# Optimization experiments

Measured on AMD Instinct MI355X. Metric: run time of the kernel, lower is better.

Reference implementation:

```python
import jax, jax.numpy as jnp
import numpy as np

N, IN_DIM, H1, H2, LIN, MAX_INDEX = 16384, 64, 256, 256, 64, 256


def _init_layer(key, out_dim, in_dim):
    # mimic kaiming_uniform(a=sqrt(5)) + uniform bias bound = 1/sqrt(fan_in)
    kW, kb = jax.random.split(key)
    bound_w = 1.0 / np.sqrt(in_dim)  # gain*sqrt(3/fan_in) with a=sqrt(5) -> 1/sqrt(fan_in)
    W = jax.random.uniform(kW, (MAX_INDEX, out_dim, in_dim), jnp.float32, -bound_w, bound_w)
    b = jax.random.uniform(kb, (MAX_INDEX, out_dim), jnp.float32, -bound_w, bound_w)
    return W, b


def setup_inputs() -> dict:
    key = jax.random.key(0)
    kx, ki, k1, k2, k3 = jax.random.split(key, 5)
    x = jax.random.normal(kx, (N, IN_DIM), jnp.float32)
    ind = jax.random.randint(ki, (N,), 0, MAX_INDEX, jnp.int64 if jax.config.jax_enable_x64 else jnp.int32)
    W1, b1 = _init_layer(k1, H1, IN_DIM)
    W2, b2 = _init_layer(k2, H2, H1)
    Wl, bl = _init_layer(k3, LIN, H2)
    return {"x": x, "ind": ind, "W1": W1, "b1": b1, "W2": W2, "b2": b2, "Wl": Wl, "bl": bl}


def _index_linear(x, ind, W, b):
    # per-row expert weight gather then row-wise matvec: out[n] = W[ind[n]] @ x[n] + b[ind[n]]
    return jnp.einsum('noi,ni->no', W[ind], x) + b[ind]


def reference(x, ind, W1, b1, W2, b2, Wl, bl):
    h = jnp.tanh(_index_linear(x, ind, W1, b1))
    h = jnp.tanh(_index_linear(h, ind, W2, b2))
    return _index_linear(h, ind, Wl, bl)
```

## Files before the change

kernel.cpp:

```cpp
#include <hip/hip_runtime.h>
#include <math.h>

#define NROWS   16384
#define IN_DIM  64
#define HID     256
#define OUT_DIM 64
#define NEXP    256
#define MT      112
#define NT      7
#define HP      264

typedef __attribute__((ext_vector_type(8))) short short8;
typedef __attribute__((ext_vector_type(4))) float f32x4;
typedef __attribute__((ext_vector_type(4))) unsigned uint4v;
typedef __attribute__((ext_vector_type(2))) unsigned uint2v;

#define LBAR() do { \
    asm volatile("s_waitcnt lgkmcnt(0)" ::: "memory"); \
    __builtin_amdgcn_s_barrier(); } while (0)


__global__ __launch_bounds__(256) void hist_k(const int* __restrict__ ind,
                                              int* __restrict__ hist) {
  int n = blockIdx.x * 256 + threadIdx.x;
  atomicAdd(&hist[ind[n]], 1);
}

__global__ __launch_bounds__(256) void scan_k(const int* __restrict__ hist,
                                              int* __restrict__ offsets,
                                              int* __restrict__ cur) {
  __shared__ int s[NEXP];
  int t = threadIdx.x;
  int h = hist[t];
  s[t] = h;
  __syncthreads();
  for (int d = 1; d < NEXP; d <<= 1) {
    int v = (t >= d) ? s[t - d] : 0;
    __syncthreads();
    s[t] += v;
    __syncthreads();
  }
  int exc = s[t] - h;
  offsets[t] = exc;
  cur[t] = exc;
  if (t == NEXP - 1) offsets[NEXP] = s[t];
}

__global__ __launch_bounds__(256) void scatter_k(const int* __restrict__ ind,
                                                 int* __restrict__ cur,
                                                 int* __restrict__ rows) {
  int n = blockIdx.x * 256 + threadIdx.x;
  int p = atomicAdd(&cur[ind[n]], 1);
  rows[p] = n;
}


__device__ __forceinline__ unsigned bf16_rn(float f) {
  unsigned u = __builtin_bit_cast(unsigned, f);
  unsigned r = 0x7fffu + ((u >> 16) & 1u);
  return (u + r) >> 16;
}

__device__ __forceinline__ unsigned pk2(float a, float b) {
  return bf16_rn(a) | (bf16_rn(b) << 16);
}

__device__ __forceinline__ short8 cvt8(f32x4 w0, f32x4 w1) {
  uint4v u;
  u.x = pk2(w0.x, w0.y);
  u.y = pk2(w0.z, w0.w);
  u.z = pk2(w1.x, w1.y);
  u.w = pk2(w1.z, w1.w);
  return __builtin_bit_cast(short8, u);
}

__device__ __forceinline__ float fast_tanh(float v) {
  float e = __expf(2.f * v);
  return 1.f - 2.f * __builtin_amdgcn_rcpf(e + 1.f);
}


__device__ __forceinline__ void preload2(const float* bp0, const float* bp1,
                                         f32x4 (&p)[2][2]) {
  p[0][0] = *(const f32x4*)(bp0);
  p[0][1] = *(const f32x4*)(bp0 + 4);
  p[1][0] = *(const f32x4*)(bp1);
  p[1][1] = *(const f32x4*)(bp1 + 4);
}

__device__ __forceinline__ void layer1_direct(const float* bp0, const float* bp1,
                                              f32x4 (&pre)[2][2],
                                              const unsigned short* Hin,
                                              int l15, int q, f32x4 (&acc)[2][NT]) {
  f32x4 wp[2][2][2];
  wp[0][0][0] = pre[0][0]; wp[0][0][1] = pre[0][1];
  wp[0][1][0] = pre[1][0]; wp[0][1][1] = pre[1][1];
#pragma unroll
  for (int ks = 0; ks < 2; ks++) {
    const int cu = ks & 1;
    if (ks + 1 < 2) {
      wp[cu ^ 1][0][0] = *(const f32x4*)(bp0 + (ks + 1) * 32);
      wp[cu ^ 1][0][1] = *(const f32x4*)(bp0 + (ks + 1) * 32 + 4);
      wp[cu ^ 1][1][0] = *(const f32x4*)(bp1 + (ks + 1) * 32);
      wp[cu ^ 1][1][1] = *(const f32x4*)(bp1 + (ks + 1) * 32 + 4);
    }
    short8 a0 = cvt8(wp[cu][0][0], wp[cu][0][1]);
    short8 a1 = cvt8(wp[cu][1][0], wp[cu][1][1]);
#pragma unroll
    for (int nt = 0; nt < NT; nt++) {
      short8 b = *(const short8*)&Hin[(nt * 16 + l15) * HP + ks * 32 + q * 8];
      acc[0][nt] = __builtin_amdgcn_mfma_f32_16x16x32_bf16(a0, b, acc[0][nt], 0, 0, 0);
      acc[1][nt] = __builtin_amdgcn_mfma_f32_16x16x32_bf16(a1, b, acc[1][nt], 0, 0, 0);
    }
  }
}

__device__ __forceinline__ void layer2_direct(const float* bp0, const float* bp1,
                                              f32x4 (&pre)[2][2][2],
                                              const unsigned short* Hin,
                                              int l15, int q, f32x4 (&acc)[2][NT]) {
  f32x4 wp[3][2][2];
  wp[0][0][0] = pre[0][0][0]; wp[0][0][1] = pre[0][0][1];
  wp[0][1][0] = pre[0][1][0]; wp[0][1][1] = pre[0][1][1];
  wp[1][0][0] = pre[1][0][0]; wp[1][0][1] = pre[1][0][1];
  wp[1][1][0] = pre[1][1][0]; wp[1][1][1] = pre[1][1][1];
#pragma unroll
  for (int ks = 0; ks < 8; ks++) {
    const int cu = ks % 3;
    const int ld = (ks + 2) % 3;
    if (ks + 2 < 8) {
      wp[ld][0][0] = *(const f32x4*)(bp0 + (ks + 2) * 32);
      wp[ld][0][1] = *(const f32x4*)(bp0 + (ks + 2) * 32 + 4);
      wp[ld][1][0] = *(const f32x4*)(bp1 + (ks + 2) * 32);
      wp[ld][1][1] = *(const f32x4*)(bp1 + (ks + 2) * 32 + 4);
    }
    short8 a0 = cvt8(wp[cu][0][0], wp[cu][0][1]);
    short8 a1 = cvt8(wp[cu][1][0], wp[cu][1][1]);
#pragma unroll
    for (int nt = 0; nt < NT; nt++) {
      short8 b = *(const short8*)&Hin[(nt * 16 + l15) * HP + ks * 32 + q * 8];
      acc[0][nt] = __builtin_amdgcn_mfma_f32_16x16x32_bf16(a0, b, acc[0][nt], 0, 0, 0);
      acc[1][nt] = __builtin_amdgcn_mfma_f32_16x16x32_bf16(a1, b, acc[1][nt], 0, 0, 0);
    }
  }
}

__device__ __forceinline__ void layer3_direct(const float* bp, f32x4 (&pre)[2],
                                              const unsigned short* Hin,
                                              int w, int l15, int q,
                                              f32x4 (&accl)[4]) {
  f32x4 wp[2][2];
  wp[0][0] = pre[0]; wp[0][1] = pre[1];
#pragma unroll
  for (int kk = 0; kk < 8; kk++) {
    const int cu = kk & 1;
    if (kk + 1 < 8) {
      wp[cu ^ 1][0] = *(const f32x4*)(bp + (kk + 1) * 32);
      wp[cu ^ 1][1] = *(const f32x4*)(bp + (kk + 1) * 32 + 4);
    }
    short8 a = cvt8(wp[cu][0], wp[cu][1]);
#pragma unroll
    for (int i = 0; i < 4; i++) {
      int nt = (w >> 2) * 4 + i;
      if (nt < NT) {
        short8 b = *(const short8*)&Hin[(nt * 16 + l15) * HP + kk * 32 + q * 8];
        accl[i] = __builtin_amdgcn_mfma_f32_16x16x32_bf16(a, b, accl[i], 0, 0, 0);
      }
    }
  }
}

__device__ __forceinline__ void write_h8(f32x4 (&acc)[2][NT], unsigned short* Hd,
                                         int w, int l15, int q) {
#pragma unroll
  for (int mt = 0; mt < 2; mt++)
#pragma unroll
    for (int nt = 0; nt < NT; nt++) {
      uint2v v;
      v.x = pk2(fast_tanh(acc[mt][nt].x), fast_tanh(acc[mt][nt].y));
      v.y = pk2(fast_tanh(acc[mt][nt].z), fast_tanh(acc[mt][nt].w));
      *(uint2v*)&Hd[(nt * 16 + l15) * HP + w * 32 + mt * 16 + q * 4] = v;
    }
}


__global__ __launch_bounds__(512, 2) void mlp_k(
    const float* __restrict__ x,
    const float* __restrict__ W1, const float* __restrict__ b1,
    const float* __restrict__ W2, const float* __restrict__ b2,
    const float* __restrict__ Wl, const float* __restrict__ bl,
    const int* __restrict__ rows, const int* __restrict__ offsets,
    float* __restrict__ out) {
  __shared__ __align__(16) unsigned short H[MT * HP];

  const int t = threadIdx.x;
  const int w = t >> 6;
  const int l15 = t & 15;
  const int q = (t >> 4) & 3;
  const int e = blockIdx.x;
  const int beg = offsets[e];
  const int cnt = offsets[e + 1] - beg;

  const float* W1e = W1 + (size_t)e * HID * IN_DIM;
  const float* W2e = W2 + (size_t)e * HID * HID;
  const float* Wle = Wl + (size_t)e * OUT_DIM * HID;

  const float* bp1a = W1e + (size_t)(w * 32 + l15) * IN_DIM + q * 8;
  const float* bp1b = W1e + (size_t)(w * 32 + 16 + l15) * IN_DIM + q * 8;
  const float* bp2a = W2e + (size_t)(w * 32 + l15) * HID + q * 8;
  const float* bp2b = W2e + (size_t)(w * 32 + 16 + l15) * HID + q * 8;
  const float* bp3  = Wle + (size_t)((w & 3) * 16 + l15) * HID + q * 8;

  f32x4 b1v[2], b2v[2], blv;
#pragma unroll
  for (int mt = 0; mt < 2; mt++) {
    b1v[mt] = *(const f32x4*)(b1 + (size_t)e * HID + w * 32 + mt * 16 + q * 4);
    b2v[mt] = *(const f32x4*)(b2 + (size_t)e * HID + w * 32 + mt * 16 + q * 4);
  }
  blv = *(const f32x4*)(bl + (size_t)e * OUT_DIM + (w & 3) * 16 + q * 4);

  const int sr = t >> 2;
  const int sc = (t & 3) * 16;

  for (int mt0 = 0; mt0 < cnt; mt0 += MT) {
    f32x4 p1[2][2], p2[2][2][2], p3[2];
    preload2(bp1a, bp1b, p1);
    preload2(bp2a, bp2b, p2[0]);
    preload2(bp2a + 32, bp2b + 32, p2[1]);
    p3[0] = *(const f32x4*)(bp3);
    p3[1] = *(const f32x4*)(bp3 + 4);

    if (sr < MT) {
      int gm = mt0 + sr;
      bool val = gm < cnt;
      int r = val ? rows[beg + gm] : 0;
      const float* xr = x + (size_t)r * IN_DIM + sc;
      uint4v u0, u1;
      if (val) {
        f32x4 a0 = *(const f32x4*)(xr);
        f32x4 a1 = *(const f32x4*)(xr + 4);
        f32x4 a2 = *(const f32x4*)(xr + 8);
        f32x4 a3 = *(const f32x4*)(xr + 12);
        u0.x = pk2(a0.x, a0.y); u0.y = pk2(a0.z, a0.w);
        u0.z = pk2(a1.x, a1.y); u0.w = pk2(a1.z, a1.w);
        u1.x = pk2(a2.x, a2.y); u1.y = pk2(a2.z, a2.w);
        u1.z = pk2(a3.x, a3.y); u1.w = pk2(a3.z, a3.w);
      } else {
        u0 = (uint4v){0, 0, 0, 0};
        u1 = (uint4v){0, 0, 0, 0};
      }
      *(uint4v*)&H[sr * HP + sc] = u0;
      *(uint4v*)&H[sr * HP + sc + 8] = u1;
    }
    LBAR();

    f32x4 acc[2][NT];
#pragma unroll
    for (int mt = 0; mt < 2; mt++)
#pragma unroll
      for (int nt = 0; nt < NT; nt++) acc[mt][nt] = b1v[mt];
    layer1_direct(bp1a, bp1b, p1, H, l15, q, acc);
    LBAR();
    write_h8(acc, H, w, l15, q);
    LBAR();

#pragma unroll
    for (int mt = 0; mt < 2; mt++)
#pragma unroll
      for (int nt = 0; nt < NT; nt++) acc[mt][nt] = b2v[mt];
    layer2_direct(bp2a, bp2b, p2, H, l15, q, acc);
    LBAR();
    write_h8(acc, H, w, l15, q);
    LBAR();

    f32x4 accl[4];
#pragma unroll
    for (int i = 0; i < 4; i++) accl[i] = blv;
    layer3_direct(bp3, p3, H, w, l15, q, accl);

#pragma unroll
    for (int i = 0; i < 4; i++) {
      int nt = (w >> 2) * 4 + i;
      if (nt < NT) {
        int gm = mt0 + nt * 16 + l15;
        if (gm < cnt) {
          int r = rows[beg + gm];
          *(f32x4*)(out + (size_t)r * OUT_DIM + (w & 3) * 16 + q * 4) = accl[i];
        }
      }
    }
    LBAR();
  }
}


extern "C" void kernel_launch(void* const* d_in, const int* in_sizes, int n_in,
                              void* d_out, int out_size, void* d_ws, size_t ws_size,
                              hipStream_t stream) {
  const float* x   = (const float*)d_in[0];
  const int*   ind = (const int*)d_in[1];
  const float* W1  = (const float*)d_in[2];
  const float* b1  = (const float*)d_in[3];
  const float* W2  = (const float*)d_in[4];
  const float* b2  = (const float*)d_in[5];
  const float* Wl  = (const float*)d_in[6];
  const float* bl  = (const float*)d_in[7];
  float* out = (float*)d_out;

  int* offsets = (int*)d_ws;
  int* cur     = (int*)d_ws + 260;
  int* hist    = (int*)d_ws + 260;
  int* rows    = (int*)d_ws + 516;

  hipMemsetAsync(hist, 0, NEXP * sizeof(int), stream);
  hist_k<<<NROWS / 256, 256, 0, stream>>>(ind, hist);
  scan_k<<<1, 256, 0, stream>>>(hist, offsets, cur);
  scatter_k<<<NROWS / 256, 256, 0, stream>>>(ind, cur, rows);
  mlp_k<<<NEXP, 512, 0, stream>>>(x, W1, b1, W2, b2, Wl, bl, rows, offsets, out);
}
```

Baseline: 163.5 us.

## Use 16 waves per expert block, each owning 16 output rows

Doubles the block to 1024 threads (16 waves), so each wave computes a single 16-row slice of the hidden outputs instead of two 32-row tiles. The row tile grows from 112 to 128 so that the average of 64 rows per expert almost always fits in one tile. Weight register pressure per thread is halved and more waves hide global-load latency, but barrier costs grow with more waves. Each B fragment read from LDS is now reused by one MFMA instead of two, which doubles LDS read traffic per FLOP.

Result: slower. 169.1 us (+3.5%).

```diff
diff --git a/kernel.cpp b/kernel.cpp
--- a/kernel.cpp
+++ b/kernel.cpp
@@ -6,8 +6,8 @@
 #define HID     256
 #define OUT_DIM 64
 #define NEXP    256
-#define MT      112
-#define NT      7
+#define MT      128
+#define NT      8
 #define HP      264
 
 typedef __attribute__((ext_vector_type(8))) short short8;
@@ -80,77 +80,38 @@
 }
 
 
-__device__ __forceinline__ void preload2(const float* bp0, const float* bp1,
-                                         f32x4 (&p)[2][2]) {
-  p[0][0] = *(const f32x4*)(bp0);
-  p[0][1] = *(const f32x4*)(bp0 + 4);
-  p[1][0] = *(const f32x4*)(bp1);
-  p[1][1] = *(const f32x4*)(bp1 + 4);
-}
-
-__device__ __forceinline__ void layer1_direct(const float* bp0, const float* bp1,
-                                              f32x4 (&pre)[2][2],
-                                              const unsigned short* Hin,
-                                              int l15, int q, f32x4 (&acc)[2][NT]) {
-  f32x4 wp[2][2][2];
-  wp[0][0][0] = pre[0][0]; wp[0][0][1] = pre[0][1];
-  wp[0][1][0] = pre[1][0]; wp[0][1][1] = pre[1][1];
-#pragma unroll
-  for (int ks = 0; ks < 2; ks++) {
-    const int cu = ks & 1;
-    if (ks + 1 < 2) {
-      wp[cu ^ 1][0][0] = *(const f32x4*)(bp0 + (ks + 1) * 32);
-      wp[cu ^ 1][0][1] = *(const f32x4*)(bp0 + (ks + 1) * 32 + 4);
-      wp[cu ^ 1][1][0] = *(const f32x4*)(bp1 + (ks + 1) * 32);
-      wp[cu ^ 1][1][1] = *(const f32x4*)(bp1 + (ks + 1) * 32 + 4);
-    }
-    short8 a0 = cvt8(wp[cu][0][0], wp[cu][0][1]);
-    short8 a1 = cvt8(wp[cu][1][0], wp[cu][1][1]);
+template <int K>
+__device__ __forceinline__ void layerN(const float* bp, f32x4 (&pre)[2][2],
+                                       const unsigned short* Hin,
+                                       int l15, int q, f32x4 (&acc)[NT]) {
+  f32x4 wp[3][2];
+  wp[0][0] = pre[0][0]; wp[0][1] = pre[0][1];
+  wp[1][0] = pre[1][0]; wp[1][1] = pre[1][1];
+  constexpr int KS = K / 32;
+#pragma unroll
+  for (int ks = 0; ks < KS; ks++) {
+    const int cu = ks % 3;
+    const int ld = (ks + 2) % 3;
+    if (ks + 2 < KS) {
+      wp[ld][0] = *(const f32x4*)(bp + (ks + 2) * 32);
+      wp[ld][1] = *(const f32x4*)(bp + (ks + 2) * 32 + 4);
+    }
+    short8 a = cvt8(wp[cu][0], wp[cu][1]);
 #pragma unroll
     for (int nt = 0; nt < NT; nt++) {
       short8 b = *(const short8*)&Hin[(nt * 16 + l15) * HP + ks * 32 + q * 8];
-      acc[0][nt] = __builtin_amdgcn_mfma_f32_16x16x32_bf16(a0, b, acc[0][nt], 0, 0, 0);
-      acc[1][nt] = __builtin_amdgcn_mfma_f32_16x16x32_bf16(a1, b, acc[1][nt], 0, 0, 0);
-    }
-  }
-}
-
-__device__ __forceinline__ void layer2_direct(const float* bp0, const float* bp1,
-                                              f32x4 (&pre)[2][2][2],
-                                              const unsigned short* Hin,
-                                              int l15, int q, f32x4 (&acc)[2][NT]) {
-  f32x4 wp[3][2][2];
-  wp[0][0][0] = pre[0][0][0]; wp[0][0][1] = pre[0][0][1];
-  wp[0][1][0] = pre[0][1][0]; wp[0][1][1] = pre[0][1][1];
-  wp[1][0][0] = pre[1][0][0]; wp[1][0][1] = pre[1][0][1];
-  wp[1][1][0] = pre[1][1][0]; wp[1][1][1] = pre[1][1][1];
-#pragma unroll
-  for (int ks = 0; ks < 8; ks++) {
-    const int cu = ks % 3;
-    const int ld = (ks + 2) % 3;
-    if (ks + 2 < 8) {
-      wp[ld][0][0] = *(const f32x4*)(bp0 + (ks + 2) * 32);
-      wp[ld][0][1] = *(const f32x4*)(bp0 + (ks + 2) * 32 + 4);
-      wp[ld][1][0] = *(const f32x4*)(bp1 + (ks + 2) * 32);
-      wp[ld][1][1] = *(const f32x4*)(bp1 + (ks + 2) * 32 + 4);
-    }
-    short8 a0 = cvt8(wp[cu][0][0], wp[cu][0][1]);
-    short8 a1 = cvt8(wp[cu][1][0], wp[cu][1][1]);
-#pragma unroll
-    for (int nt = 0; nt < NT; nt++) {
-      short8 b = *(const short8*)&Hin[(nt * 16 + l15) * HP + ks * 32 + q * 8];
-      acc[0][nt] = __builtin_amdgcn_mfma_f32_16x16x32_bf16(a0, b, acc[0][nt], 0, 0, 0);
-      acc[1][nt] = __builtin_amdgcn_mfma_f32_16x16x32_bf16(a1, b, acc[1][nt], 0, 0, 0);
-    }
-  }
-}
-
-__device__ __forceinline__ void layer3_direct(const float* bp, f32x4 (&pre)[2],
-                                              const unsigned short* Hin,
-                                              int w, int l15, int q,
-                                              f32x4 (&accl)[4]) {
+      acc[nt] = __builtin_amdgcn_mfma_f32_16x16x32_bf16(a, b, acc[nt], 0, 0, 0);
+    }
+  }
+}
+
+__device__ __forceinline__ void layer3_16(const float* bp, f32x4 (&pre)[2],
+                                          const unsigned short* Hin,
+                                          int w, int l15, int q,
+                                          f32x4 (&accl)[2]) {
   f32x4 wp[2][2];
   wp[0][0] = pre[0]; wp[0][1] = pre[1];
+  const int rt = w >> 2;
 #pragma unroll
   for (int kk = 0; kk < 8; kk++) {
     const int cu = kk & 1;
@@ -160,31 +121,27 @@
     }
     short8 a = cvt8(wp[cu][0], wp[cu][1]);
 #pragma unroll
-    for (int i = 0; i < 4; i++) {
-      int nt = (w >> 2) * 4 + i;
-      if (nt < NT) {
-        short8 b = *(const short8*)&Hin[(nt * 16 + l15) * HP + kk * 32 + q * 8];
-        accl[i] = __builtin_amdgcn_mfma_f32_16x16x32_bf16(a, b, accl[i], 0, 0, 0);
-      }
-    }
-  }
-}
-
-__device__ __forceinline__ void write_h8(f32x4 (&acc)[2][NT], unsigned short* Hd,
-                                         int w, int l15, int q) {
-#pragma unroll
-  for (int mt = 0; mt < 2; mt++)
-#pragma unroll
-    for (int nt = 0; nt < NT; nt++) {
-      uint2v v;
-      v.x = pk2(fast_tanh(acc[mt][nt].x), fast_tanh(acc[mt][nt].y));
-      v.y = pk2(fast_tanh(acc[mt][nt].z), fast_tanh(acc[mt][nt].w));
-      *(uint2v*)&Hd[(nt * 16 + l15) * HP + w * 32 + mt * 16 + q * 4] = v;
-    }
-}
-
-
-__global__ __launch_bounds__(512, 2) void mlp_k(
+    for (int i = 0; i < 2; i++) {
+      int nt = rt * 2 + i;
+      short8 b = *(const short8*)&Hin[(nt * 16 + l15) * HP + kk * 32 + q * 8];
+      accl[i] = __builtin_amdgcn_mfma_f32_16x16x32_bf16(a, b, accl[i], 0, 0, 0);
+    }
+  }
+}
+
+__device__ __forceinline__ void write_h16(f32x4 (&acc)[NT], unsigned short* Hd,
+                                          int w, int l15, int q) {
+#pragma unroll
+  for (int nt = 0; nt < NT; nt++) {
+    uint2v v;
+    v.x = pk2(fast_tanh(acc[nt].x), fast_tanh(acc[nt].y));
+    v.y = pk2(fast_tanh(acc[nt].z), fast_tanh(acc[nt].w));
+    *(uint2v*)&Hd[(nt * 16 + l15) * HP + w * 16 + q * 4] = v;
+  }
+}
+
+
+__global__ __launch_bounds__(1024, 4) void mlp_k(
     const float* __restrict__ x,
     const float* __restrict__ W1, const float* __restrict__ b1,
     const float* __restrict__ W2, const float* __restrict__ b2,
@@ -205,88 +162,73 @@
   const float* W2e = W2 + (size_t)e * HID * HID;
   const float* Wle = Wl + (size_t)e * OUT_DIM * HID;
 
-  const float* bp1a = W1e + (size_t)(w * 32 + l15) * IN_DIM + q * 8;
-  const float* bp1b = W1e + (size_t)(w * 32 + 16 + l15) * IN_DIM + q * 8;
-  const float* bp2a = W2e + (size_t)(w * 32 + l15) * HID + q * 8;
-  const float* bp2b = W2e + (size_t)(w * 32 + 16 + l15) * HID + q * 8;
-  const float* bp3  = Wle + (size_t)((w & 3) * 16 + l15) * HID + q * 8;
-
-  f32x4 b1v[2], b2v[2], blv;
-#pragma unroll
-  for (int mt = 0; mt < 2; mt++) {
-    b1v[mt] = *(const f32x4*)(b1 + (size_t)e * HID + w * 32 + mt * 16 + q * 4);
-    b2v[mt] = *(const f32x4*)(b2 + (size_t)e * HID + w * 32 + mt * 16 + q * 4);
-  }
-  blv = *(const f32x4*)(bl + (size_t)e * OUT_DIM + (w & 3) * 16 + q * 4);
-
-  const int sr = t >> 2;
-  const int sc = (t & 3) * 16;
+  const float* bp1 = W1e + (size_t)(w * 16 + l15) * IN_DIM + q * 8;
+  const float* bp2 = W2e + (size_t)(w * 16 + l15) * HID + q * 8;
+  const float* bp3 = Wle + (size_t)((w & 3) * 16 + l15) * HID + q * 8;
+
+  const f32x4 b1v = *(const f32x4*)(b1 + (size_t)e * HID + w * 16 + q * 4);
+  const f32x4 b2v = *(const f32x4*)(b2 + (size_t)e * HID + w * 16 + q * 4);
+  const f32x4 blv = *(const f32x4*)(bl + (size_t)e * OUT_DIM + (w & 3) * 16 + q * 4);
+
+  const int sr = t >> 3;
+  const int sc = (t & 7) * 8;
 
   for (int mt0 = 0; mt0 < cnt; mt0 += MT) {
-    f32x4 p1[2][2], p2[2][2][2], p3[2];
-    preload2(bp1a, bp1b, p1);
-    preload2(bp2a, bp2b, p2[0]);
-    preload2(bp2a + 32, bp2b + 32, p2[1]);
+    f32x4 p1[2][2], p2[2][2], p3[2];
+#pragma unroll
+    for (int k = 0; k < 2; k++) {
+      p1[k][0] = *(const f32x4*)(bp1 + k * 32);
+      p1[k][1] = *(const f32x4*)(bp1 + k * 32 + 4);
+      p2[k][0] = *(const f32x4*)(bp2 + k * 32);
+      p2[k][1] = *(const f32x4*)(bp2 + k * 32 + 4);
+    }
     p3[0] = *(const f32x4*)(bp3);
     p3[1] = *(const f32x4*)(bp3 + 4);
 
-    if (sr < MT) {
+    {
       int gm = mt0 + sr;
       bool val = gm < cnt;
       int r = val ? rows[beg + gm] : 0;
       const float* xr = x + (size_t)r * IN_DIM + sc;
-      uint4v u0, u1;
+      uint4v u;
       if (val) {
         f32x4 a0 = *(const f32x4*)(xr);
         f32x4 a1 = *(const f32x4*)(xr + 4);
-        f32x4 a2 = *(const f32x4*)(xr + 8);
-        f32x4 a3 = *(const f32x4*)(xr + 12);
-        u0.x = pk2(a0.x, a0.y); u0.y = pk2(a0.z, a0.w);
-        u0.z = pk2(a1.x, a1.y); u0.w = pk2(a1.z, a1.w);
-        u1.x = pk2(a2.x, a2.y); u1.y = pk2(a2.z, a2.w);
-        u1.z = pk2(a3.x, a3.y); u1.w = pk2(a3.z, a3.w);
+        u.x = pk2(a0.x, a0.y); u.y = pk2(a0.z, a0.w);
+        u.z = pk2(a1.x, a1.y); u.w = pk2(a1.z, a1.w);
       } else {
-        u0 = (uint4v){0, 0, 0, 0};
-        u1 = (uint4v){0, 0, 0, 0};
+        u = (uint4v){0, 0, 0, 0};
       }
-      *(uint4v*)&H[sr * HP + sc] = u0;
-      *(uint4v*)&H[sr * HP + sc + 8] = u1;
-    }
-    LBAR();
-
-    f32x4 acc[2][NT];
-#pragma unroll
-    for (int mt = 0; mt < 2; mt++)
-#pragma unroll
-      for (int nt = 0; nt < NT; nt++) acc[mt][nt] = b1v[mt];
-    layer1_direct(bp1a, bp1b, p1, H, l15, q, acc);
-    LBAR();
-    write_h8(acc, H, w, l15, q);
-    LBAR();
-
-#pragma unroll
-    for (int mt = 0; mt < 2; mt++)
-#pragma unroll
-      for (int nt = 0; nt < NT; nt++) acc[mt][nt] = b2v[mt];
-    layer2_direct(bp2a, bp2b, p2, H, l15, q, acc);
-    LBAR();
-    write_h8(acc, H, w, l15, q);
-    LBAR();
-
-    f32x4 accl[4];
-#pragma unroll
-    for (int i = 0; i < 4; i++) accl[i] = blv;
-    layer3_direct(bp3, p3, H, w, l15, q, accl);
-
-#pragma unroll
-    for (int i = 0; i < 4; i++) {
-      int nt = (w >> 2) * 4 + i;
-      if (nt < NT) {
-        int gm = mt0 + nt * 16 + l15;
-        if (gm < cnt) {
-          int r = rows[beg + gm];
-          *(f32x4*)(out + (size_t)r * OUT_DIM + (w & 3) * 16 + q * 4) = accl[i];
-        }
+      *(uint4v*)&H[sr * HP + sc] = u;
+    }
+    LBAR();
+
+    f32x4 acc[NT];
+#pragma unroll
+    for (int nt = 0; nt < NT; nt++) acc[nt] = b1v;
+    layerN<IN_DIM>(bp1, p1, H, l15, q, acc);
+    LBAR();
+    write_h16(acc, H, w, l15, q);
+    LBAR();
+
+#pragma unroll
+    for (int nt = 0; nt < NT; nt++) acc[nt] = b2v;
+    layerN<HID>(bp2, p2, H, l15, q, acc);
+    LBAR();
+    write_h16(acc, H, w, l15, q);
+    LBAR();
+
+    f32x4 accl[2];
+    accl[0] = blv; accl[1] = blv;
+    layer3_16(bp3, p3, H, w, l15, q, accl);
+
+#pragma unroll
+    for (int i = 0; i < 2; i++) {
+      int nt = (w >> 2) * 2 + i;
+      int gm = mt0 + nt * 16 + l15;
+      if (gm < cnt) {
+        int r = rows[beg + gm];
+        *(f32x4*)(out + (size_t)r * OUT_DIM + (w & 3) * 16 + q * 4) = accl[i];
       }
     }
     LBAR();
@@ -316,5 +258,5 @@
   hist_k<<<NROWS / 256, 256, 0, stream>>>(ind, hist);
   scan_k<<<1, 256, 0, stream>>>(hist, offsets, cur);
   scatter_k<<<NROWS / 256, 256, 0, stream>>>(ind, cur, rows);
-  mlp_k<<<NEXP, 512, 0, stream>>>(x, W1, b1, W2, b2, Wl, bl, rows, offsets, out);
-}
+  mlp_k<<<NEXP, 1024, 0, stream>>>(x, W1, b1, W2, b2, Wl, bl, rows, offsets, out);
+}
```

## Prefetch expert weights deeper across layer phases into register arrays

Applied to the files above, without the earlier changes.

Changes the weight-loading schedule from a per-k-step rolling prefetch to bulk loads into full per-layer register arrays. Layer-2 and layer-3 weight loads are issued early: half of layer 2 before layer 1 runs, the rest during layer 1, and layer 3 in the middle of layer 2. The x row loads are also issued ahead of the weight loads. The aim is to hide global memory latency behind MFMA work and barriers. In exchange, register use rises sharply (P2 alone holds 32 f32x4 values), which may lower occupancy or cause spills.

New measurement: 169.0 us. 3.4% more time.

```diff
diff --git a/kernel.cpp b/kernel.cpp
--- a/kernel.cpp
+++ b/kernel.cpp
@@ -80,32 +80,45 @@
 }
 
 
-__device__ __forceinline__ void preload2(const float* bp0, const float* bp1,
-                                         f32x4 (&p)[2][2]) {
-  p[0][0] = *(const f32x4*)(bp0);
-  p[0][1] = *(const f32x4*)(bp0 + 4);
-  p[1][0] = *(const f32x4*)(bp1);
-  p[1][1] = *(const f32x4*)(bp1 + 4);
-}
-
-__device__ __forceinline__ void layer1_direct(const float* bp0, const float* bp1,
-                                              f32x4 (&pre)[2][2],
-                                              const unsigned short* Hin,
-                                              int l15, int q, f32x4 (&acc)[2][NT]) {
-  f32x4 wp[2][2][2];
-  wp[0][0][0] = pre[0][0]; wp[0][0][1] = pre[0][1];
-  wp[0][1][0] = pre[1][0]; wp[0][1][1] = pre[1][1];
+__device__ __forceinline__ void loadP1(const float* bp0, const float* bp1,
+                                       f32x4 (&P)[2][2][2]) {
 #pragma unroll
   for (int ks = 0; ks < 2; ks++) {
-    const int cu = ks & 1;
-    if (ks + 1 < 2) {
-      wp[cu ^ 1][0][0] = *(const f32x4*)(bp0 + (ks + 1) * 32);
-      wp[cu ^ 1][0][1] = *(const f32x4*)(bp0 + (ks + 1) * 32 + 4);
-      wp[cu ^ 1][1][0] = *(const f32x4*)(bp1 + (ks + 1) * 32);
-      wp[cu ^ 1][1][1] = *(const f32x4*)(bp1 + (ks + 1) * 32 + 4);
-    }
-    short8 a0 = cvt8(wp[cu][0][0], wp[cu][0][1]);
-    short8 a1 = cvt8(wp[cu][1][0], wp[cu][1][1]);
+    P[ks][0][0] = *(const f32x4*)(bp0 + ks * 32);
+    P[ks][0][1] = *(const f32x4*)(bp0 + ks * 32 + 4);
+    P[ks][1][0] = *(const f32x4*)(bp1 + ks * 32);
+    P[ks][1][1] = *(const f32x4*)(bp1 + ks * 32 + 4);
+  }
+}
+
+template <int LO, int HI>
+__device__ __forceinline__ void loadP2(const float* bp0, const float* bp1,
+                                       f32x4 (&P)[8][2][2]) {
+#pragma unroll
+  for (int ks = LO; ks < HI; ks++) {
+    P[ks][0][0] = *(const f32x4*)(bp0 + ks * 32);
+    P[ks][0][1] = *(const f32x4*)(bp0 + ks * 32 + 4);
+    P[ks][1][0] = *(const f32x4*)(bp1 + ks * 32);
+    P[ks][1][1] = *(const f32x4*)(bp1 + ks * 32 + 4);
+  }
+}
+
+template <int LO, int HI>
+__device__ __forceinline__ void loadP3(const float* bp, f32x4 (&P)[8][2]) {
+#pragma unroll
+  for (int kk = LO; kk < HI; kk++) {
+    P[kk][0] = *(const f32x4*)(bp + kk * 32);
+    P[kk][1] = *(const f32x4*)(bp + kk * 32 + 4);
+  }
+}
+
+__device__ __forceinline__ void l1_compute(const f32x4 (&P)[2][2][2],
+                                           const unsigned short* Hin,
+                                           int l15, int q, f32x4 (&acc)[2][NT]) {
+#pragma unroll
+  for (int ks = 0; ks < 2; ks++) {
+    short8 a0 = cvt8(P[ks][0][0], P[ks][0][1]);
+    short8 a1 = cvt8(P[ks][1][0], P[ks][1][1]);
 #pragma unroll
     for (int nt = 0; nt < NT; nt++) {
       short8 b = *(const short8*)&Hin[(nt * 16 + l15) * HP + ks * 32 + q * 8];
@@ -115,27 +128,14 @@
   }
 }
 
-__device__ __forceinline__ void layer2_direct(const float* bp0, const float* bp1,
-                                              f32x4 (&pre)[2][2][2],
-                                              const unsigned short* Hin,
-                                              int l15, int q, f32x4 (&acc)[2][NT]) {
-  f32x4 wp[3][2][2];
-  wp[0][0][0] = pre[0][0][0]; wp[0][0][1] = pre[0][0][1];
-  wp[0][1][0] = pre[0][1][0]; wp[0][1][1] = pre[0][1][1];
-  wp[1][0][0] = pre[1][0][0]; wp[1][0][1] = pre[1][0][1];
-  wp[1][1][0] = pre[1][1][0]; wp[1][1][1] = pre[1][1][1];
-#pragma unroll
-  for (int ks = 0; ks < 8; ks++) {
-    const int cu = ks % 3;
-    const int ld = (ks + 2) % 3;
-    if (ks + 2 < 8) {
-      wp[ld][0][0] = *(const f32x4*)(bp0 + (ks + 2) * 32);
-      wp[ld][0][1] = *(const f32x4*)(bp0 + (ks + 2) * 32 + 4);
-      wp[ld][1][0] = *(const f32x4*)(bp1 + (ks + 2) * 32);
-      wp[ld][1][1] = *(const f32x4*)(bp1 + (ks + 2) * 32 + 4);
-    }
-    short8 a0 = cvt8(wp[cu][0][0], wp[cu][0][1]);
-    short8 a1 = cvt8(wp[cu][1][0], wp[cu][1][1]);
+template <int LO, int HI>
+__device__ __forceinline__ void l2_compute(const f32x4 (&P)[8][2][2],
+                                           const unsigned short* Hin,
+                                           int l15, int q, f32x4 (&acc)[2][NT]) {
+#pragma unroll
+  for (int ks = LO; ks < HI; ks++) {
+    short8 a0 = cvt8(P[ks][0][0], P[ks][0][1]);
+    short8 a1 = cvt8(P[ks][1][0], P[ks][1][1]);
 #pragma unroll
     for (int nt = 0; nt < NT; nt++) {
       short8 b = *(const short8*)&Hin[(nt * 16 + l15) * HP + ks * 32 + q * 8];
@@ -145,20 +145,13 @@
   }
 }
 
-__device__ __forceinline__ void layer3_direct(const float* bp, f32x4 (&pre)[2],
-                                              const unsigned short* Hin,
-                                              int w, int l15, int q,
-                                              f32x4 (&accl)[4]) {
-  f32x4 wp[2][2];
-  wp[0][0] = pre[0]; wp[0][1] = pre[1];
+__device__ __forceinline__ void l3_compute(const f32x4 (&P)[8][2],
+                                           const unsigned short* Hin,
+                                           int w, int l15, int q,
+                                           f32x4 (&accl)[4]) {
 #pragma unroll
   for (int kk = 0; kk < 8; kk++) {
-    const int cu = kk & 1;
-    if (kk + 1 < 8) {
-      wp[cu ^ 1][0] = *(const f32x4*)(bp + (kk + 1) * 32);
-      wp[cu ^ 1][1] = *(const f32x4*)(bp + (kk + 1) * 32 + 4);
-    }
-    short8 a = cvt8(wp[cu][0], wp[cu][1]);
+    short8 a = cvt8(P[kk][0], P[kk][1]);
 #pragma unroll
     for (int i = 0; i < 4; i++) {
       int nt = (w >> 2) * 4 + i;
@@ -223,24 +216,31 @@
   const int sc = (t & 3) * 16;
 
   for (int mt0 = 0; mt0 < cnt; mt0 += MT) {
-    f32x4 p1[2][2], p2[2][2][2], p3[2];
-    preload2(bp1a, bp1b, p1);
-    preload2(bp2a, bp2b, p2[0]);
-    preload2(bp2a + 32, bp2b + 32, p2[1]);
-    p3[0] = *(const f32x4*)(bp3);
-    p3[1] = *(const f32x4*)(bp3 + 4);
-
+    f32x4 a0, a1, a2, a3;
+    bool val = false;
     if (sr < MT) {
       int gm = mt0 + sr;
-      bool val = gm < cnt;
+      val = gm < cnt;
       int r = val ? rows[beg + gm] : 0;
       const float* xr = x + (size_t)r * IN_DIM + sc;
+      if (val) {
+        a0 = *(const f32x4*)(xr);
+        a1 = *(const f32x4*)(xr + 4);
+        a2 = *(const f32x4*)(xr + 8);
+        a3 = *(const f32x4*)(xr + 12);
+      }
+    }
+
+    f32x4 P1[2][2][2];
+    f32x4 P2[8][2][2];
+    f32x4 P3[8][2];
+    loadP1(bp1a, bp1b, P1);
+    loadP2<0, 4>(bp2a, bp2b, P2);
+    loadP3<0, 2>(bp3, P3);
+
+    if (sr < MT) {
       uint4v u0, u1;
       if (val) {
-        f32x4 a0 = *(const f32x4*)(xr);
-        f32x4 a1 = *(const f32x4*)(xr + 4);
-        f32x4 a2 = *(const f32x4*)(xr + 8);
-        f32x4 a3 = *(const f32x4*)(xr + 12);
         u0.x = pk2(a0.x, a0.y); u0.y = pk2(a0.z, a0.w);
         u0.z = pk2(a1.x, a1.y); u0.w = pk2(a1.z, a1.w);
         u1.x = pk2(a2.x, a2.y); u1.y = pk2(a2.z, a2.w);
@@ -254,12 +254,13 @@
     }
     LBAR();
 
+    loadP2<4, 8>(bp2a, bp2b, P2);
     f32x4 acc[2][NT];
 #pragma unroll
     for (int mt = 0; mt < 2; mt++)
 #pragma unroll
       for (int nt = 0; nt < NT; nt++) acc[mt][nt] = b1v[mt];
-    layer1_direct(bp1a, bp1b, p1, H, l15, q, acc);
+    l1_compute(P1, H, l15, q, acc);
     LBAR();
     write_h8(acc, H, w, l15, q);
     LBAR();
@@ -268,7 +269,9 @@
     for (int mt = 0; mt < 2; mt++)
 #pragma unroll
       for (int nt = 0; nt < NT; nt++) acc[mt][nt] = b2v[mt];
-    layer2_direct(bp2a, bp2b, p2, H, l15, q, acc);
+    l2_compute<0, 4>(P2, H, l15, q, acc);
+    loadP3<2, 8>(bp3, P3);
+    l2_compute<4, 8>(P2, H, l15, q, acc);
     LBAR();
     write_h8(acc, H, w, l15, q);
     LBAR();
@@ -276,7 +279,7 @@
     f32x4 accl[4];
 #pragma unroll
     for (int i = 0; i < 4; i++) accl[i] = blv;
-    layer3_direct(bp3, p3, H, w, l15, q, accl);
+    l3_compute(P3, H, w, l15, q, accl);
 
 #pragma unroll
     for (int i = 0; i < 4; i++) {
```
